# Performance work log

Hardware: AMD Instinct MI355X
Metric: run time of the kernel (lower is better)

## Reference

```python
import jax, jax.numpy as jnp
import numpy as np

G = 512        # graphs in batch
N_PER = 256    # nodes per graph (equal-size graphs)
D = 128        # embed_dim
E_PER = 4096   # edges per graph
KEEP = 0.5
K = int(np.ceil(KEEP * N_PER))  # 128 nodes kept per graph (PyG topk: ceil(ratio*n))
N = G * N_PER
E = G * E_PER


def setup_inputs() -> dict:
    key = jax.random.key(0)
    k1, k2, k3, k4, k5 = jax.random.split(key, 5)
    x = jax.random.normal(k1, (N, D), jnp.float32)
    offs = (jnp.arange(G, dtype=jnp.int32) * N_PER)[:, None]
    src = jax.random.randint(k2, (G, E_PER), 0, N_PER, dtype=jnp.int32) + offs
    dst = jax.random.randint(k3, (G, E_PER), 0, N_PER, dtype=jnp.int32) + offs
    edge_index = jnp.stack([src.reshape(-1), dst.reshape(-1)], axis=0)  # [2, E], within-graph edges
    graph_indicator = jnp.repeat(jnp.arange(G, dtype=jnp.int32), N_PER)  # [N]
    gcn_w = jax.random.normal(k4, (D, 1), jnp.float32) / np.sqrt(D)
    gcn_b = jnp.zeros((1,), jnp.float32)
    lin_w = jax.random.normal(k5, (2 * D, D), jnp.float32) / np.sqrt(2 * D)
    lin_b = jnp.zeros((D,), jnp.float32)
    return {"input_feature": x, "graph_indicator": graph_indicator, "edge_index": edge_index,
            "gcn_w": gcn_w, "gcn_b": gcn_b, "lin_w": lin_w, "lin_b": lin_b}


def gcn_conv(x, edge_index, w, b):
    # PyG GCNConv: add self-loops, symmetric normalization, aggregate at target (edge_index[1]).
    n = x.shape[0]
    loop = jnp.arange(n, dtype=edge_index.dtype)
    row = jnp.concatenate([edge_index[0], loop])  # source
    col = jnp.concatenate([edge_index[1], loop])  # target
    deg = jax.ops.segment_sum(jnp.ones_like(col, dtype=x.dtype), col, num_segments=n)
    dinv = jax.lax.rsqrt(deg)  # deg >= 1 due to self-loops
    norm = dinv[row] * dinv[col]            # [E+N]
    xw = x @ w                              # [N, out]
    msg = xw[row] * norm[:, None]           # gather + scale
    agg = jax.ops.segment_sum(msg, col, num_segments=n)
    return agg + b


def reference(input_feature, graph_indicator, edge_index, gcn_w, gcn_b, lin_w, lin_b):
    # SAGPool: attention scores via GCNConv(d -> 1)
    score = gcn_conv(input_feature, edge_index, gcn_w, gcn_b).squeeze(-1)  # [N]
    # per-graph top-k mask (equal-size graphs -> reshape)
    s = score.reshape(G, N_PER)
    _, idx = jax.lax.top_k(s, K)                                          # [G, K]
    mask = jnp.zeros((G, N_PER), bool).at[jnp.arange(G)[:, None], idx].set(True)
    # gated features of kept nodes: x[mask] * tanh(score[mask])
    feat = (input_feature * jnp.tanh(score)[:, None]).reshape(G, N_PER, D)
    m = mask[..., None]
    # global mean/max pool over kept nodes per graph (exactly K kept per graph)
    mean = jnp.sum(jnp.where(m, feat, 0.0), axis=1) / K                   # [G, D]
    mx = jnp.max(jnp.where(m, feat, -jnp.inf), axis=1)                    # [G, D]
    readout = jnp.concatenate([mean, mx], axis=1)                         # [G, 2D]
    return readout @ lin_w + lin_b                                        # [G, D]
```

## Files before the change

kernel.cpp:

```cpp
#include <hip/hip_runtime.h>
#include <math.h>

#define NG   512
#define NPER 256
#define DD   128
#define EPER 4096
#define KK   128
#define NT   512
#define NW   8

__global__ __launch_bounds__(NT, 4) void sag_fused(
    const float* __restrict__ x,
    const int*   __restrict__ esrc,
    const int*   __restrict__ edst,
    const float* __restrict__ gcn_w,
    const float* __restrict__ gcn_b,
    const float* __restrict__ lin_w,
    const float* __restrict__ lin_b,
    float* __restrict__ out)
{
  const int g    = blockIdx.x;
  const int tid  = threadIdx.x;
  const int lane = tid & 63;
  const int wave = tid >> 6;

  __shared__ float  sXW[NPER];
  __shared__ float  sXWn[NPER];
  __shared__ float  sDinv[NPER];
  __shared__ int    sDeg[NPER];
  __shared__ int    sRank[NPER];
  __shared__ float4 sScore4[NPER / 4];
  __shared__ int2   sKG[KK];
  __shared__ float2 sPS[NW][64];
  __shared__ float2 sPM[NW][64];
  __shared__ float2 sR2[DD];
  float* sScore = (float*)sScore4;

  const int4* es4 = (const int4*)(esrc + (size_t)g * EPER);
  const int4* ed4 = (const int4*)(edst + (size_t)g * EPER);
  int4 sa = es4[tid], sb = es4[NT + tid];
  int4 da = ed4[tid], db = ed4[NT + tid];

  if (tid < NPER) { sDeg[tid] = 1; sRank[tid] = 0; }
  __syncthreads();

  const float*  xg  = x + (size_t)g * NPER * DD;
  const float4* xg4 = (const float4*)xg;
  const int j   = lane & 15;
  const int sub = lane >> 4;
  float4 wa = ((const float4*)gcn_w)[j];
  float4 wb = ((const float4*)gcn_w)[16 + j];
  #pragma unroll
  for (int r = 0; r < 8; ++r) {
    int node = r * 32 + wave * 4 + sub;
    float4 q0 = xg4[node * 32 + j];
    float4 q1 = xg4[node * 32 + 16 + j];
    float acc = q0.x*wa.x + q0.y*wa.y + q0.z*wa.z + q0.w*wa.w
              + q1.x*wb.x + q1.y*wb.y + q1.z*wb.z + q1.w*wb.w;
    acc += __shfl_xor(acc, 1);
    acc += __shfl_xor(acc, 2);
    acc += __shfl_xor(acc, 4);
    acc += __shfl_xor(acc, 8);
    if (j == 0) sXW[node] = acc;
  }
  atomicAdd(&sDeg[da.x & 255], 1);
  atomicAdd(&sDeg[da.y & 255], 1);
  atomicAdd(&sDeg[da.z & 255], 1);
  atomicAdd(&sDeg[da.w & 255], 1);
  atomicAdd(&sDeg[db.x & 255], 1);
  atomicAdd(&sDeg[db.y & 255], 1);
  atomicAdd(&sDeg[db.z & 255], 1);
  atomicAdd(&sDeg[db.w & 255], 1);
  __syncthreads();

  if (tid < NPER) {
    float dv  = 1.0f / sqrtf((float)sDeg[tid]);
    float xwn = sXW[tid] * dv;
    sDinv[tid]  = dv;
    sXWn[tid]   = xwn;
    sScore[tid] = xwn * dv;
  }
  __syncthreads();

  {
    int s0 = sa.x & 255, d0 = da.x & 255;
    int s1 = sa.y & 255, d1 = da.y & 255;
    int s2 = sa.z & 255, d2 = da.z & 255;
    int s3 = sa.w & 255, d3 = da.w & 255;
    int s4 = sb.x & 255, d4 = db.x & 255;
    int s5 = sb.y & 255, d5 = db.y & 255;
    int s6 = sb.z & 255, d6 = db.z & 255;
    int s7 = sb.w & 255, d7 = db.w & 255;
    atomicAdd(&sScore[d0], sXWn[s0] * sDinv[d0]);
    atomicAdd(&sScore[d1], sXWn[s1] * sDinv[d1]);
    atomicAdd(&sScore[d2], sXWn[s2] * sDinv[d2]);
    atomicAdd(&sScore[d3], sXWn[s3] * sDinv[d3]);
    atomicAdd(&sScore[d4], sXWn[s4] * sDinv[d4]);
    atomicAdd(&sScore[d5], sXWn[s5] * sDinv[d5]);
    atomicAdd(&sScore[d6], sXWn[s6] * sDinv[d6]);
    atomicAdd(&sScore[d7], sXWn[s7] * sDinv[d7]);
  }
  __syncthreads();

  {
    int node = tid & 255;
    int seg  = tid >> 8;
    float s_i = sScore[node];
    int base = seg * 32;
    int part = 0;
    #pragma unroll 8
    for (int t = 0; t < 32; ++t) {
      float4 v = sScore4[base + t];
      int jj = (base + t) * 4;
      part += (v.x > s_i) || (v.x == s_i && (jj + 0) < node);
      part += (v.y > s_i) || (v.y == s_i && (jj + 1) < node);
      part += (v.z > s_i) || (v.z == s_i && (jj + 2) < node);
      part += (v.w > s_i) || (v.w == s_i && (jj + 3) < node);
    }
    atomicAdd(&sRank[node], part);
  }
  __syncthreads();
  {
    const float bval = gcn_b[0];
    if (tid < NPER) {
      int r = sRank[tid];
      if (r < KK) sKG[r] = make_int2(tid, __float_as_int(tanhf(sScore[tid] + bval)));
    }
  }
  __syncthreads();

  const float2* xg2 = (const float2*)xg;
  float sm0 = 0.f, sm1 = 0.f, mx0 = -INFINITY, mx1 = -INFINITY;
  #pragma unroll
  for (int t = 0; t < 16; ++t) {
    int2 kg = sKG[wave * 16 + t];
    float gt = __int_as_float(kg.y);
    float2 p = xg2[kg.x * 64 + lane];
    float a = p.x * gt, b = p.y * gt;
    sm0 += a; sm1 += b;
    mx0 = fmaxf(mx0, a); mx1 = fmaxf(mx1, b);
  }
  sPS[wave][lane] = make_float2(sm0, sm1);
  sPM[wave][lane] = make_float2(mx0, mx1);
  __syncthreads();
  if (wave == 0) {
    float2 a = sPS[0][lane];
    #pragma unroll
    for (int w = 1; w < NW; ++w) { float2 p = sPS[w][lane]; a.x += p.x; a.y += p.y; }
    sR2[lane] = make_float2(a.x * (1.0f / KK), a.y * (1.0f / KK));
  } else if (wave == 1) {
    float2 a = sPM[0][lane];
    #pragma unroll
    for (int w = 1; w < NW; ++w) {
      float2 p = sPM[w][lane];
      a.x = fmaxf(a.x, p.x); a.y = fmaxf(a.y, p.y);
    }
    sR2[64 + lane] = a;
  }
  __syncthreads();

  const float2* lw2 = (const float2*)lin_w;
  float a0 = 0.f, a1 = 0.f;
  #pragma unroll
  for (int t = 0; t < 16; ++t) {
    int k2 = wave * 16 + t;
    float2 rv = sR2[k2];
    float2 p0 = lw2[(2 * k2) * 64 + lane];
    float2 p1 = lw2[(2 * k2 + 1) * 64 + lane];
    a0 += rv.x * p0.x + rv.y * p1.x;
    a1 += rv.x * p0.y + rv.y * p1.y;
  }
  sPS[wave][lane] = make_float2(a0, a1);
  __syncthreads();
  if (wave == 0) {
    float2 a = sPS[0][lane];
    #pragma unroll
    for (int w = 1; w < NW; ++w) { float2 p = sPS[w][lane]; a.x += p.x; a.y += p.y; }
    float2 bb = ((const float2*)lin_b)[lane];
    a.x += bb.x; a.y += bb.y;
    ((float2*)out)[(size_t)g * 64 + lane] = a;
  }
}

extern "C" void kernel_launch(void* const* d_in, const int* in_sizes, int n_in,
                              void* d_out, int out_size, void* d_ws, size_t ws_size,
                              hipStream_t stream) {
  const float* x  = (const float*)d_in[0];
  const int*   ei = (const int*)d_in[2];
  const float* gw = (const float*)d_in[3];
  const float* gb = (const float*)d_in[4];
  const float* lw = (const float*)d_in[5];
  const float* lb = (const float*)d_in[6];
  float* out = (float*)d_out;
  const int E = in_sizes[2] / 2;
  sag_fused<<<NG, NT, 0, stream>>>(x, ei, ei + E, gw, gb, lw, lb, out);
}
```

Measured before the change: 128.8 us.

## Split fused SAGPool kernel into projection, scoring and pooling kernels

Replaces the single per-graph fused kernel with three launches. A wide node-parallel kernel computes x·w, a per-graph kernel computes degrees, scores, ranks and writes a gate/keep flag per node to workspace, and a pooling kernel streams all node rows with masked mean/max before the final linear layer. The aim is to expose more parallelism and memory-level concurrency in the projection and to remove the serial chain inside one block. In exchange, x is read twice in full, workspace traffic is added, and there are two extra kernel launches.

```diff
diff --git a/kernel.cpp b/kernel.cpp
--- a/kernel.cpp
+++ b/kernel.cpp
@@ -6,63 +6,63 @@
 #define DD   128
 #define EPER 4096
 #define KK   128
-#define NT   512
-#define NW   8
-
-__global__ __launch_bounds__(NT, 4) void sag_fused(
-    const float* __restrict__ x,
-    const int*   __restrict__ esrc,
-    const int*   __restrict__ edst,
-    const float* __restrict__ gcn_w,
-    const float* __restrict__ gcn_b,
-    const float* __restrict__ lin_w,
-    const float* __restrict__ lin_b,
-    float* __restrict__ out)
+#define NN   (NG * NPER)
+
+__global__ __launch_bounds__(256, 4) void k_xw(
+    const float* __restrict__ x, const float* __restrict__ gcn_w,
+    float* __restrict__ xw)
 {
-  const int g    = blockIdx.x;
   const int tid  = threadIdx.x;
   const int lane = tid & 63;
   const int wave = tid >> 6;
-
-  __shared__ float  sXW[NPER];
+  const int r    = lane >> 2;
+  const int q    = lane & 3;
+  const int node = blockIdx.x * 64 + wave * 16 + r;
+
+  const float4* x4 = (const float4*)x;
+  const float4* w4 = (const float4*)gcn_w;
+
+  float4 wv[8], qv[8];
+  #pragma unroll
+  for (int i = 0; i < 8; ++i) wv[i] = w4[i * 4 + q];
+  #pragma unroll
+  for (int i = 0; i < 8; ++i) qv[i] = x4[node * 32 + i * 4 + q];
+
+  float acc = 0.f;
+  #pragma unroll
+  for (int i = 0; i < 8; ++i)
+    acc += qv[i].x * wv[i].x + qv[i].y * wv[i].y
+         + qv[i].z * wv[i].z + qv[i].w * wv[i].w;
+  acc += __shfl_xor(acc, 1);
+  acc += __shfl_xor(acc, 2);
+  if (q == 0) xw[node] = acc;
+}
+
+__global__ __launch_bounds__(512, 4) void k_score(
+    const float* __restrict__ xw,
+    const int*   __restrict__ esrc, const int* __restrict__ edst,
+    const float* __restrict__ gcn_b,
+    float2* __restrict__ gateflag)
+{
+  const int g   = blockIdx.x;
+  const int tid = threadIdx.x;
+
+  __shared__ int    sDeg[NPER];
+  __shared__ int    sRank[NPER];
   __shared__ float  sXWn[NPER];
   __shared__ float  sDinv[NPER];
-  __shared__ int    sDeg[NPER];
-  __shared__ int    sRank[NPER];
   __shared__ float4 sScore4[NPER / 4];
-  __shared__ int2   sKG[KK];
-  __shared__ float2 sPS[NW][64];
-  __shared__ float2 sPM[NW][64];
-  __shared__ float2 sR2[DD];
   float* sScore = (float*)sScore4;
 
   const int4* es4 = (const int4*)(esrc + (size_t)g * EPER);
   const int4* ed4 = (const int4*)(edst + (size_t)g * EPER);
-  int4 sa = es4[tid], sb = es4[NT + tid];
-  int4 da = ed4[tid], db = ed4[NT + tid];
+  int4 sa = es4[tid], sb = es4[512 + tid];
+  int4 da = ed4[tid], db = ed4[512 + tid];
+  float xwv = (tid < NPER) ? xw[(size_t)g * NPER + tid] : 0.f;
 
   if (tid < NPER) { sDeg[tid] = 1; sRank[tid] = 0; }
   __syncthreads();
 
-  const float*  xg  = x + (size_t)g * NPER * DD;
-  const float4* xg4 = (const float4*)xg;
-  const int j   = lane & 15;
-  const int sub = lane >> 4;
-  float4 wa = ((const float4*)gcn_w)[j];
-  float4 wb = ((const float4*)gcn_w)[16 + j];
-  #pragma unroll
-  for (int r = 0; r < 8; ++r) {
-    int node = r * 32 + wave * 4 + sub;
-    float4 q0 = xg4[node * 32 + j];
-    float4 q1 = xg4[node * 32 + 16 + j];
-    float acc = q0.x*wa.x + q0.y*wa.y + q0.z*wa.z + q0.w*wa.w
-              + q1.x*wb.x + q1.y*wb.y + q1.z*wb.z + q1.w*wb.w;
-    acc += __shfl_xor(acc, 1);
-    acc += __shfl_xor(acc, 2);
-    acc += __shfl_xor(acc, 4);
-    acc += __shfl_xor(acc, 8);
-    if (j == 0) sXW[node] = acc;
-  }
   atomicAdd(&sDeg[da.x & 255], 1);
   atomicAdd(&sDeg[da.y & 255], 1);
   atomicAdd(&sDeg[da.z & 255], 1);
@@ -74,11 +74,10 @@
   __syncthreads();
 
   if (tid < NPER) {
-    float dv  = 1.0f / sqrtf((float)sDeg[tid]);
-    float xwn = sXW[tid] * dv;
+    float dv = 1.0f / sqrtf((float)sDeg[tid]);
     sDinv[tid]  = dv;
-    sXWn[tid]   = xwn;
-    sScore[tid] = xwn * dv;
+    sXWn[tid]   = xwv * dv;
+    sScore[tid] = xwv * dv * dv;
   }
   __syncthreads();
 
@@ -120,38 +119,61 @@
     atomicAdd(&sRank[node], part);
   }
   __syncthreads();
-  {
-    const float bval = gcn_b[0];
-    if (tid < NPER) {
-      int r = sRank[tid];
-      if (r < KK) sKG[r] = make_int2(tid, __float_as_int(tanhf(sScore[tid] + bval)));
-    }
-  }
-  __syncthreads();
-
-  const float2* xg2 = (const float2*)xg;
+
+  if (tid < NPER) {
+    int rk = sRank[tid];
+    float2 gf = (rk < KK)
+        ? make_float2(tanhf(sScore[tid] + gcn_b[0]), 1.0f)
+        : make_float2(0.f, 0.f);
+    gateflag[(size_t)g * NPER + tid] = gf;
+  }
+}
+
+__global__ __launch_bounds__(512, 4) void k_pool(
+    const float*  __restrict__ x,
+    const float2* __restrict__ gateflag,
+    const float*  __restrict__ lin_w, const float* __restrict__ lin_b,
+    float* __restrict__ out)
+{
+  const int g    = blockIdx.x;
+  const int tid  = threadIdx.x;
+  const int lane = tid & 63;
+  const int wave = tid >> 6;
+
+  __shared__ float2 sGF[NPER];
+  __shared__ float2 sPS[8][64];
+  __shared__ float2 sPM[8][64];
+  __shared__ float2 sR2[DD];
+
+  if (tid < NPER) sGF[tid] = gateflag[(size_t)g * NPER + tid];
+  __syncthreads();
+
+  const float2* xg2 = (const float2*)(x + (size_t)g * NPER * DD);
   float sm0 = 0.f, sm1 = 0.f, mx0 = -INFINITY, mx1 = -INFINITY;
   #pragma unroll
-  for (int t = 0; t < 16; ++t) {
-    int2 kg = sKG[wave * 16 + t];
-    float gt = __int_as_float(kg.y);
-    float2 p = xg2[kg.x * 64 + lane];
-    float a = p.x * gt, b = p.y * gt;
+  for (int nn = 0; nn < 32; ++nn) {
+    int node = wave * 32 + nn;
+    float2 gf = sGF[node];
+    float2 p  = xg2[node * 64 + lane];
+    bool kp = (gf.y != 0.f);
+    float a = p.x * gf.x, b = p.y * gf.x;
     sm0 += a; sm1 += b;
-    mx0 = fmaxf(mx0, a); mx1 = fmaxf(mx1, b);
+    mx0 = fmaxf(mx0, kp ? a : -INFINITY);
+    mx1 = fmaxf(mx1, kp ? b : -INFINITY);
   }
   sPS[wave][lane] = make_float2(sm0, sm1);
   sPM[wave][lane] = make_float2(mx0, mx1);
   __syncthreads();
+
   if (wave == 0) {
     float2 a = sPS[0][lane];
     #pragma unroll
-    for (int w = 1; w < NW; ++w) { float2 p = sPS[w][lane]; a.x += p.x; a.y += p.y; }
+    for (int w = 1; w < 8; ++w) { float2 p = sPS[w][lane]; a.x += p.x; a.y += p.y; }
     sR2[lane] = make_float2(a.x * (1.0f / KK), a.y * (1.0f / KK));
   } else if (wave == 1) {
     float2 a = sPM[0][lane];
     #pragma unroll
-    for (int w = 1; w < NW; ++w) {
+    for (int w = 1; w < 8; ++w) {
       float2 p = sPM[w][lane];
       a.x = fmaxf(a.x, p.x); a.y = fmaxf(a.y, p.y);
     }
@@ -175,7 +197,7 @@
   if (wave == 0) {
     float2 a = sPS[0][lane];
     #pragma unroll
-    for (int w = 1; w < NW; ++w) { float2 p = sPS[w][lane]; a.x += p.x; a.y += p.y; }
+    for (int w = 1; w < 8; ++w) { float2 p = sPS[w][lane]; a.x += p.x; a.y += p.y; }
     float2 bb = ((const float2*)lin_b)[lane];
     a.x += bb.x; a.y += bb.y;
     ((float2*)out)[(size_t)g * 64 + lane] = a;
@@ -193,5 +215,11 @@
   const float* lb = (const float*)d_in[6];
   float* out = (float*)d_out;
   const int E = in_sizes[2] / 2;
-  sag_fused<<<NG, NT, 0, stream>>>(x, ei, ei + E, gw, gb, lw, lb, out);
-}
+
+  float*  xw = (float*)d_ws;
+  float2* gf = (float2*)((char*)d_ws + (size_t)NN * 4);
+
+  k_xw   <<<NN / 64, 256, 0, stream>>>(x, gw, xw);
+  k_score<<<NG, 512, 0, stream>>>(xw, ei, ei + E, gb, gf);
+  k_pool <<<NG, 512, 0, stream>>>(x, gf, lw, lb, out);
+}
```

After: 143.3 us. 11.3% more time.

## Keep graph features in registers and pool over all nodes with masks

Applied to the files above, without the earlier changes.

Each thread now loads its 16 floats for 8 nodes of x into registers up front, before the degree atomics, and reuses them for both the x·w projection and the final mean/max pooling. The second gather of the kept nodes' rows from global memory goes away. Pooling now covers all 256 nodes, with a per-node gate that is zero for dropped nodes and an infinite offset that removes them from the max, followed by shuffle and shared-memory reductions. This trades the global re-read and the sKG compaction for higher register pressure (64 floats of x per thread), which may lower occupancy under launch_bounds(512,4), plus twice the pooling arithmetic.

```diff
diff --git a/kernel.cpp b/kernel.cpp
--- a/kernel.cpp
+++ b/kernel.cpp
@@ -23,46 +23,40 @@
   const int tid  = threadIdx.x;
   const int lane = tid & 63;
   const int wave = tid >> 6;
-
-  __shared__ float  sXW[NPER];
+  const int j    = lane & 15;
+  const int sub  = lane >> 4;
+
+  __shared__ int    sDeg[NPER];
+  __shared__ int    sRank[NPER];
   __shared__ float  sXWn[NPER];
   __shared__ float  sDinv[NPER];
-  __shared__ int    sDeg[NPER];
-  __shared__ int    sRank[NPER];
   __shared__ float4 sScore4[NPER / 4];
-  __shared__ int2   sKG[KK];
-  __shared__ float2 sPS[NW][64];
-  __shared__ float2 sPM[NW][64];
+  __shared__ float2 sGF[NPER];
+  __shared__ float  sPoolS[NW][DD];
+  __shared__ float  sPoolM[NW][DD];
   __shared__ float2 sR2[DD];
   float* sScore = (float*)sScore4;
+  float* sR     = (float*)sR2;
 
   const int4* es4 = (const int4*)(esrc + (size_t)g * EPER);
   const int4* ed4 = (const int4*)(edst + (size_t)g * EPER);
   int4 sa = es4[tid], sb = es4[NT + tid];
   int4 da = ed4[tid], db = ed4[NT + tid];
 
-  if (tid < NPER) { sDeg[tid] = 1; sRank[tid] = 0; }
-  __syncthreads();
-
-  const float*  xg  = x + (size_t)g * NPER * DD;
-  const float4* xg4 = (const float4*)xg;
-  const int j   = lane & 15;
-  const int sub = lane >> 4;
+  const float4* xg4 = (const float4*)(x + (size_t)g * NPER * DD);
+  const int colbase = (wave * 4 + sub) * 32 + j;
+  float4 q0[8], q1[8];
+  #pragma unroll
+  for (int r = 0; r < 8; ++r) {
+    q0[r] = xg4[r * 1024 + colbase];
+    q1[r] = xg4[r * 1024 + colbase + 16];
+  }
   float4 wa = ((const float4*)gcn_w)[j];
   float4 wb = ((const float4*)gcn_w)[16 + j];
-  #pragma unroll
-  for (int r = 0; r < 8; ++r) {
-    int node = r * 32 + wave * 4 + sub;
-    float4 q0 = xg4[node * 32 + j];
-    float4 q1 = xg4[node * 32 + 16 + j];
-    float acc = q0.x*wa.x + q0.y*wa.y + q0.z*wa.z + q0.w*wa.w
-              + q1.x*wb.x + q1.y*wb.y + q1.z*wb.z + q1.w*wb.w;
-    acc += __shfl_xor(acc, 1);
-    acc += __shfl_xor(acc, 2);
-    acc += __shfl_xor(acc, 4);
-    acc += __shfl_xor(acc, 8);
-    if (j == 0) sXW[node] = acc;
-  }
+
+  if (tid < NPER) { sDeg[tid] = 1; sRank[tid] = 0; }
+  __syncthreads();
+
   atomicAdd(&sDeg[da.x & 255], 1);
   atomicAdd(&sDeg[da.y & 255], 1);
   atomicAdd(&sDeg[da.z & 255], 1);
@@ -71,14 +65,25 @@
   atomicAdd(&sDeg[db.y & 255], 1);
   atomicAdd(&sDeg[db.z & 255], 1);
   atomicAdd(&sDeg[db.w & 255], 1);
+
+  #pragma unroll
+  for (int r = 0; r < 8; ++r) {
+    float acc = q0[r].x*wa.x + q0[r].y*wa.y + q0[r].z*wa.z + q0[r].w*wa.w
+              + q1[r].x*wb.x + q1[r].y*wb.y + q1[r].z*wb.z + q1[r].w*wb.w;
+    acc += __shfl_xor(acc, 1);
+    acc += __shfl_xor(acc, 2);
+    acc += __shfl_xor(acc, 4);
+    acc += __shfl_xor(acc, 8);
+    if (j == 0) sXWn[r * 32 + wave * 4 + sub] = acc;
+  }
   __syncthreads();
 
   if (tid < NPER) {
-    float dv  = 1.0f / sqrtf((float)sDeg[tid]);
-    float xwn = sXW[tid] * dv;
+    float dv = 1.0f / sqrtf((float)sDeg[tid]);
+    float xw = sXWn[tid];
     sDinv[tid]  = dv;
-    sXWn[tid]   = xwn;
-    sScore[tid] = xwn * dv;
+    sXWn[tid]   = xw * dv;
+    sScore[tid] = xw * dv * dv;
   }
   __syncthreads();
 
@@ -120,42 +125,56 @@
     atomicAdd(&sRank[node], part);
   }
   __syncthreads();
-  {
-    const float bval = gcn_b[0];
-    if (tid < NPER) {
-      int r = sRank[tid];
-      if (r < KK) sKG[r] = make_int2(tid, __float_as_int(tanhf(sScore[tid] + bval)));
-    }
-  }
-  __syncthreads();
-
-  const float2* xg2 = (const float2*)xg;
-  float sm0 = 0.f, sm1 = 0.f, mx0 = -INFINITY, mx1 = -INFINITY;
-  #pragma unroll
-  for (int t = 0; t < 16; ++t) {
-    int2 kg = sKG[wave * 16 + t];
-    float gt = __int_as_float(kg.y);
-    float2 p = xg2[kg.x * 64 + lane];
-    float a = p.x * gt, b = p.y * gt;
-    sm0 += a; sm1 += b;
-    mx0 = fmaxf(mx0, a); mx1 = fmaxf(mx1, b);
-  }
-  sPS[wave][lane] = make_float2(sm0, sm1);
-  sPM[wave][lane] = make_float2(mx0, mx1);
-  __syncthreads();
-  if (wave == 0) {
-    float2 a = sPS[0][lane];
+
+  if (tid < NPER) {
+    bool kp = sRank[tid] < KK;
+    float gate = tanhf(sScore[tid] + gcn_b[0]);
+    sGF[tid] = make_float2(kp ? gate : 0.0f, kp ? 0.0f : INFINITY);
+  }
+  __syncthreads();
+
+  float su0=0,su1=0,su2=0,su3=0,su4=0,su5=0,su6=0,su7=0;
+  float mx0=-INFINITY,mx1=-INFINITY,mx2=-INFINITY,mx3=-INFINITY;
+  float mx4=-INFINITY,mx5=-INFINITY,mx6=-INFINITY,mx7=-INFINITY;
+  #pragma unroll
+  for (int r = 0; r < 8; ++r) {
+    float2 gf = sGF[r * 32 + wave * 4 + sub];
+    float g1 = gf.x, fb = gf.y;
+    float a;
+    a = q0[r].x * g1; su0 += a; mx0 = fmaxf(mx0, a - fb);
+    a = q0[r].y * g1; su1 += a; mx1 = fmaxf(mx1, a - fb);
+    a = q0[r].z * g1; su2 += a; mx2 = fmaxf(mx2, a - fb);
+    a = q0[r].w * g1; su3 += a; mx3 = fmaxf(mx3, a - fb);
+    a = q1[r].x * g1; su4 += a; mx4 = fmaxf(mx4, a - fb);
+    a = q1[r].y * g1; su5 += a; mx5 = fmaxf(mx5, a - fb);
+    a = q1[r].z * g1; su6 += a; mx6 = fmaxf(mx6, a - fb);
+    a = q1[r].w * g1; su7 += a; mx7 = fmaxf(mx7, a - fb);
+  }
+  #define RED_S(v) v += __shfl_xor(v,16); v += __shfl_xor(v,32);
+  #define RED_M(v) v = fmaxf(v,__shfl_xor(v,16)); v = fmaxf(v,__shfl_xor(v,32));
+  RED_S(su0) RED_S(su1) RED_S(su2) RED_S(su3)
+  RED_S(su4) RED_S(su5) RED_S(su6) RED_S(su7)
+  RED_M(mx0) RED_M(mx1) RED_M(mx2) RED_M(mx3)
+  RED_M(mx4) RED_M(mx5) RED_M(mx6) RED_M(mx7)
+  if (sub == 0) {
+    ((float4*)&sPoolS[wave][4 * j])[0]      = make_float4(su0, su1, su2, su3);
+    ((float4*)&sPoolS[wave][64 + 4 * j])[0] = make_float4(su4, su5, su6, su7);
+    ((float4*)&sPoolM[wave][4 * j])[0]      = make_float4(mx0, mx1, mx2, mx3);
+    ((float4*)&sPoolM[wave][64 + 4 * j])[0] = make_float4(mx4, mx5, mx6, mx7);
+  }
+  __syncthreads();
+
+  if (tid < DD) {
+    float s = 0.f;
     #pragma unroll
-    for (int w = 1; w < NW; ++w) { float2 p = sPS[w][lane]; a.x += p.x; a.y += p.y; }
-    sR2[lane] = make_float2(a.x * (1.0f / KK), a.y * (1.0f / KK));
-  } else if (wave == 1) {
-    float2 a = sPM[0][lane];
+    for (int w = 0; w < NW; ++w) s += sPoolS[w][tid];
+    sR[tid] = s * (1.0f / KK);
+  } else if (tid < 2 * DD) {
+    int d = tid - DD;
+    float m = -INFINITY;
     #pragma unroll
-    for (int w = 1; w < NW; ++w) {
-      float2 p = sPM[w][lane];
-      a.x = fmaxf(a.x, p.x); a.y = fmaxf(a.y, p.y);
-    }
-    sR2[64 + lane] = a;
+    for (int w = 0; w < NW; ++w) m = fmaxf(m, sPoolM[w][d]);
+    sR[tid] = m;
   }
   __syncthreads();
 
@@ -170,12 +189,13 @@
     a0 += rv.x * p0.x + rv.y * p1.x;
     a1 += rv.x * p0.y + rv.y * p1.y;
   }
-  sPS[wave][lane] = make_float2(a0, a1);
+  float2* sP2 = (float2*)sPoolS;
+  sP2[wave * 64 + lane] = make_float2(a0, a1);
   __syncthreads();
   if (wave == 0) {
-    float2 a = sPS[0][lane];
+    float2 a = sP2[lane];
     #pragma unroll
-    for (int w = 1; w < NW; ++w) { float2 p = sPS[w][lane]; a.x += p.x; a.y += p.y; }
+    for (int w = 1; w < NW; ++w) { float2 p = sP2[w * 64 + lane]; a.x += p.x; a.y += p.y; }
     float2 bb = ((const float2*)lin_b)[lane];
     a.x += bb.x; a.y += bb.y;
     ((float2*)out)[(size_t)g * 64 + lane] = a;
```

Result: no change. 127.7 us (-0.8%).
